# Kernel optimization log

Measured on AMD Instinct MI355X. Metric: run time of the kernel, lower is better.

## Reference

```python
import jax, jax.numpy as jnp
import numpy as np

D = 128
H = 8
HEAD_DIM = D // H
N_NODES = 50000
N_EDGES = 200000
ARGS_PER_EDGE = 3
N_ARGS = N_EDGES * ARGS_PER_EDGE  # 600000
B = N_EDGES // 2                  # 2 edges packed per sequence
S = 2 * (ARGS_PER_EDGE + 1)       # 8
N_TYPES = 512
N_ARGNAMES = 1024


def setup_inputs() -> dict:
    key = jax.random.key(0)
    ks = jax.random.split(key, 10)
    nodes_representations = jax.random.normal(ks[0], (N_NODES, D), jnp.float32)
    hyperedge_arg_node_idxs = jax.random.randint(ks[1], (N_ARGS,), 0, N_NODES)
    unq_hyperedge_type_reprs = jax.random.normal(ks[2], (N_TYPES, D), jnp.float32)
    hyperedge_type_name_unq_idxs = jax.random.randint(ks[3], (N_EDGES,), 0, N_TYPES)
    unq_hyperedge_arg_name_reprs = jax.random.normal(ks[4], (N_ARGNAMES, D), jnp.float32)
    hyperedge_arg_name_unq_idxs = jax.random.randint(ks[5], (N_ARGS,), 0, N_ARGNAMES)

    # Bucket layout: sequence i packs edges e0=2i, e1=2i+1; each edge contributes
    # its 3 arg positions then its state-token position (N_ARGS + edge_id).
    e = np.arange(N_EDGES, dtype=np.int64).reshape(B, 2)          # [B,2]
    arg_base = e * ARGS_PER_EDGE                                   # [B,2]
    per_edge = np.concatenate(
        [arg_base[..., None] + np.arange(ARGS_PER_EDGE), (N_ARGS + e)[..., None]],
        axis=-1)                                                   # [B,2,4]
    flattened_arg_idxs = jnp.asarray(per_edge.reshape(B, S))       # [B,8]
    arg_to_edge_id = jnp.asarray(np.repeat(e, ARGS_PER_EDGE + 1, axis=1))  # [B,8]

    s = 0.05
    W_arg = jax.random.normal(ks[6], (D, D), jnp.float32) * s
    b_arg = jnp.zeros((D,), jnp.float32)
    W_qkv = jax.random.normal(ks[7], (3 * D, D), jnp.float32) * s
    b_qkv = jnp.zeros((3 * D,), jnp.float32)
    W_out = jax.random.normal(ks[8], (D, D), jnp.float32) * s
    b_out = jnp.zeros((D,), jnp.float32)

    return dict(
        nodes_representations=nodes_representations,
        hyperedge_arg_node_idxs=hyperedge_arg_node_idxs,
        unq_hyperedge_type_reprs=unq_hyperedge_type_reprs,
        hyperedge_type_name_unq_idxs=hyperedge_type_name_unq_idxs,
        unq_hyperedge_arg_name_reprs=unq_hyperedge_arg_name_reprs,
        hyperedge_arg_name_unq_idxs=hyperedge_arg_name_unq_idxs,
        flattened_arg_idxs=flattened_arg_idxs,
        arg_to_edge_id=arg_to_edge_id,
        W_arg=W_arg, b_arg=b_arg, W_qkv=W_qkv, b_qkv=b_qkv,
        W_out=W_out, b_out=b_out,
    )


def reference(nodes_representations, hyperedge_arg_node_idxs, unq_hyperedge_type_reprs,
              hyperedge_type_name_unq_idxs, unq_hyperedge_arg_name_reprs,
              hyperedge_arg_name_unq_idxs, flattened_arg_idxs, arg_to_edge_id,
              W_arg, b_arg, W_qkv, b_qkv, W_out, b_out):
    # per-arg representation = gathered node repr + encoded arg-name repr
    arg_name_reprs = (unq_hyperedge_arg_name_reprs @ W_arg.T + b_arg)[hyperedge_arg_name_unq_idxs]
    arg_node_reprs = nodes_representations[hyperedge_arg_node_idxs]
    arg_reprs = arg_node_reprs + arg_name_reprs                       # [N_ARGS, D]
    edge_state_reprs = unq_hyperedge_type_reprs[hyperedge_type_name_unq_idxs]  # [N_EDGES, D]

    # concat args, states, and a trailing ones row (padding target)
    all_reprs = jnp.concatenate(
        [arg_reprs, edge_state_reprs, jnp.ones((1, D), arg_reprs.dtype)], axis=0)  # [L, D]

    x = all_reprs[flattened_arg_idxs]                                 # [B, S, D]

    # torch MultiheadAttention (batch_first, self-attention)
    qkv = x @ W_qkv.T + b_qkv                                         # [B, S, 3D]
    q, k, v = jnp.split(qkv, 3, axis=-1)
    to_heads = lambda t: t.reshape(B, S, H, HEAD_DIM).transpose(0, 2, 1, 3)
    q, k, v = to_heads(q), to_heads(k), to_heads(v)                   # [B, H, S, dh]

    scores = jnp.einsum('bhqd,bhkd->bhqk', q, k) / np.float32(np.sqrt(HEAD_DIM))
    # block-diagonal mask: disallow attention across different edge ids
    mask = arg_to_edge_id[:, :, None] != arg_to_edge_id[:, None, :]   # [B, S, S]
    scores = jnp.where(mask[:, None, :, :], -jnp.inf, scores)
    attn = jax.nn.softmax(scores, axis=-1)
    out = jnp.einsum('bhqk,bhkd->bhqd', attn, v)                      # [B, H, S, dh]
    out = out.transpose(0, 2, 1, 3).reshape(B, S, D)
    messages = out @ W_out.T + b_out                                  # [B, S, D]

    # scatter back into the flat buffer (indices are unique by construction)
    L = N_ARGS + N_EDGES + 1
    buf = jnp.zeros((L, D), messages.dtype)
    buf = buf.at[flattened_arg_idxs.reshape(-1)].set(messages.reshape(-1, D))

    messages_to_nodes = buf[:N_ARGS]
    edge_states = buf[N_ARGS:N_ARGS + N_EDGES]
    return messages_to_nodes, edge_states
```

## Files before the change

### kernel.cpp

```cpp
#include <hip/hip_runtime.h>

#define D        128
#define N_NODES  50000
#define N_EDGES  200000
#define N_ARGS   600000
#define EDGES_PER_TILE 16
#define TOK      64
#define LDX      136

typedef unsigned short u16;
typedef __bf16 bf16x8 __attribute__((ext_vector_type(8)));
typedef float  f32x4  __attribute__((ext_vector_type(4)));

#define MFMA(A,B,C) __builtin_amdgcn_mfma_f32_16x16x32_bf16((A),(B),(C),0,0,0)

#define WS_ARG   0
#define WS_TYPE  262144
#define WS_WQKV  393216
#define WS_WOUT  491520
#define WS_BQKV  524288
#define WS_BOUT  525056
#define WS_FLAG  525312

__device__ __forceinline__ float b2f(u16 h) {
    return __uint_as_float(((unsigned)h) << 16);
}
__device__ __forceinline__ u16 f2b(float f) {
    unsigned u = __float_as_uint(f);
    u += 0x7FFFu + ((u >> 16) & 1u);
    return (u16)(u >> 16);
}
__device__ __forceinline__ unsigned pack2(float lo, float hi) {
    return (unsigned)f2b(lo) | ((unsigned)f2b(hi) << 16);
}
__device__ __forceinline__ unsigned addbf2(unsigned a, unsigned b) {
    float lo = __uint_as_float(a << 16)         + __uint_as_float(b << 16);
    float hi = __uint_as_float(a & 0xFFFF0000u) + __uint_as_float(b & 0xFFFF0000u);
    return pack2(lo, hi);
}

__global__ void sniff_kernel(const u16* __restrict__ probe, int* __restrict__ flag) {
    __shared__ int cnt;
    if (threadIdx.x == 0) cnt = 0;
    __syncthreads();
    float v = b2f(probe[threadIdx.x]);
    float a = fabsf(v);
    int insane = (v != v) || (v != 0.0f && (a < 1e-5f || a > 1e5f));
    atomicAdd(&cnt, insane);
    __syncthreads();
    if (threadIdx.x == 0) *flag = (cnt > 16) ? 1 : 0;
}

__global__ void conv_kernel(const void* __restrict__ t,  const void* __restrict__ wq,
                            const void* __restrict__ wo, const void* __restrict__ bq,
                            const void* __restrict__ bo, char* __restrict__ wsc,
                            const int* __restrict__ flagp) {
    const bool f32 = (*flagp) != 0;
    int i = blockIdx.x * 256 + threadIdx.x;
    const void* src; u16* dst; int j;
    if      (i <  65536) { src = t;  dst = (u16*)(wsc + WS_TYPE); j = i; }
    else if (i < 114688) { src = wq; dst = (u16*)(wsc + WS_WQKV); j = i - 65536; }
    else if (i < 131072) { src = wo; dst = (u16*)(wsc + WS_WOUT); j = i - 114688; }
    else if (i < 131456) { src = bq; dst = (u16*)(wsc + WS_BQKV); j = i - 131072; }
    else if (i < 131584) { src = bo; dst = (u16*)(wsc + WS_BOUT); j = i - 131456; }
    else return;
    dst[j] = f32 ? f2b(((const float*)src)[j]) : ((const u16*)src)[j];
}

__global__ void argname_kernel(const void* __restrict__ unq, const void* __restrict__ W,
                               const void* __restrict__ b, u16* __restrict__ tab,
                               const int* __restrict__ flagp) {
    const bool f32 = (*flagp) != 0;
    int n = blockIdx.x;
    int d = threadIdx.x;
    __shared__ float xs[D];
    xs[d] = f32 ? ((const float*)unq)[n * D + d] : b2f(((const u16*)unq)[n * D + d]);
    __syncthreads();
    float acc = f32 ? ((const float*)b)[d] : b2f(((const u16*)b)[d]);
    if (f32) {
        const float4* wr = (const float4*)((const float*)W + d * D);
        #pragma unroll
        for (int t = 0; t < 32; ++t) {
            float4 wv = wr[t];
            const float* x = &xs[t * 4];
            acc += x[0] * wv.x + x[1] * wv.y + x[2] * wv.z + x[3] * wv.w;
        }
    } else {
        const uint4* wr = (const uint4*)((const u16*)W + d * D);
        #pragma unroll
        for (int t = 0; t < 16; ++t) {
            uint4 wv = wr[t];
            const float* x = &xs[t * 8];
            acc += x[0] * b2f((u16)(wv.x)) + x[1] * b2f((u16)(wv.x >> 16));
            acc += x[2] * b2f((u16)(wv.y)) + x[3] * b2f((u16)(wv.y >> 16));
            acc += x[4] * b2f((u16)(wv.z)) + x[5] * b2f((u16)(wv.z >> 16));
            acc += x[6] * b2f((u16)(wv.w)) + x[7] * b2f((u16)(wv.w >> 16));
        }
    }
    tab[n * D + d] = f2b(acc);
}

__global__ __launch_bounds__(256, 2)
void fused_kernel(const void* __restrict__ nodes,
                  const int*  __restrict__ nidx,
                  const int*  __restrict__ tidx,
                  const int*  __restrict__ anidx,
                  const char* __restrict__ wsc,
                  void*       __restrict__ outv,
                  const int*  __restrict__ flagp) {
    __shared__ __align__(16) u16 Xs[TOK * LDX];
    __shared__ __align__(16) u16 Os[TOK * LDX];

    const bool f32  = (*flagp) != 0;
    const u16* argtab = (const u16*)(wsc + WS_ARG);
    const u16* typetab= (const u16*)(wsc + WS_TYPE);
    const u16* Wqkv   = (const u16*)(wsc + WS_WQKV);
    const u16* Wout   = (const u16*)(wsc + WS_WOUT);
    const u16* bqkv   = (const u16*)(wsc + WS_BQKV);
    const u16* bout   = (const u16*)(wsc + WS_BOUT);

    const int tid  = threadIdx.x;
    const int tile = blockIdx.x;

    {
        int row  = tid >> 2;
        int part = tid & 3;
        int e    = tile * EDGES_PER_TILE + (row >> 2);
        int i    = row & 3;
        uint4* dst = (uint4*)&Xs[row * LDX + part * 32];
        if (i < 3) {
            int a = 3 * e + i;
            const uint4* pa = (const uint4*)(argtab + (long)anidx[a] * D + part * 32);
            if (f32) {
                const float4* pn = (const float4*)((const float*)nodes + (long)nidx[a] * D + part * 32);
                #pragma unroll
                for (int t = 0; t < 4; ++t) {
                    float4 f0 = pn[2 * t], f1 = pn[2 * t + 1];
                    uint4 ua = pa[t], r;
                    r.x = pack2(f0.x + b2f((u16)ua.x), f0.y + b2f((u16)(ua.x >> 16)));
                    r.y = pack2(f0.z + b2f((u16)ua.y), f0.w + b2f((u16)(ua.y >> 16)));
                    r.z = pack2(f1.x + b2f((u16)ua.z), f1.y + b2f((u16)(ua.z >> 16)));
                    r.w = pack2(f1.z + b2f((u16)ua.w), f1.w + b2f((u16)(ua.w >> 16)));
                    dst[t] = r;
                }
            } else {
                const uint4* pn = (const uint4*)((const u16*)nodes + (long)nidx[a] * D + part * 32);
                #pragma unroll
                for (int t = 0; t < 4; ++t) {
                    uint4 un = pn[t], ua = pa[t], r;
                    r.x = addbf2(un.x, ua.x); r.y = addbf2(un.y, ua.y);
                    r.z = addbf2(un.z, ua.z); r.w = addbf2(un.w, ua.w);
                    dst[t] = r;
                }
            }
        } else {
            const uint4* pt = (const uint4*)(typetab + (long)tidx[e] * D + part * 32);
            #pragma unroll
            for (int t = 0; t < 4; ++t) dst[t] = pt[t];
        }
    }
    __syncthreads();

    const int w    = tid >> 6;
    const int lane = tid & 63;
    const int q    = lane >> 4;
    const int c    = lane & 15;

    bf16x8 a[4][4];
    #pragma unroll
    for (int mt = 0; mt < 4; ++mt)
        #pragma unroll
        for (int kk = 0; kk < 4; ++kk)
            a[mt][kk] = *(const bf16x8*)&Xs[(mt * 16 + c) * LDX + kk * 32 + q * 8];

    const f32x4 zero = {0.f, 0.f, 0.f, 0.f};
    const bool valid = (q == (c >> 2));

    #pragma unroll
    for (int hi = 0; hi < 2; ++hi) {
        int h = 2 * w + hi;

        f32x4 QT[4], KT[4], Vv[4];
        {
            f32x4 q0, k0, v0;
            const u16* p0 = bqkv +       h * 16 + q * 4;
            const u16* p1 = bqkv + 128 + h * 16 + q * 4;
            float bv = b2f(bqkv[256 + h * 16 + c]);
            #pragma unroll
            for (int j = 0; j < 4; ++j) {
                q0[j] = b2f(p0[j]); k0[j] = b2f(p1[j]); v0[j] = bv;
            }
            #pragma unroll
            for (int mt = 0; mt < 4; ++mt) { QT[mt] = q0; KT[mt] = k0; Vv[mt] = v0; }
        }

        #pragma unroll
        for (int kk = 0; kk < 4; ++kk) {
            int ko = kk * 32 + q * 8;
            bf16x8 bq = *(const bf16x8*)(Wqkv + (long)(      h * 16 + c) * D + ko);
            bf16x8 bk = *(const bf16x8*)(Wqkv + (long)(128 + h * 16 + c) * D + ko);
            bf16x8 bv = *(const bf16x8*)(Wqkv + (long)(256 + h * 16 + c) * D + ko);
            #pragma unroll
            for (int mt = 0; mt < 4; ++mt) {
                QT[mt] = MFMA(bq, a[mt][kk], QT[mt]);
                KT[mt] = MFMA(bk, a[mt][kk], KT[mt]);
                Vv[mt] = MFMA(a[mt][kk], bv, Vv[mt]);
            }
        }

        #pragma unroll
        for (int mt = 0; mt < 4; ++mt) {
            bf16x8 qf = {}, kf = {}, vf = {};
            #pragma unroll
            for (int j = 0; j < 4; ++j) {
                qf[j] = (__bf16)QT[mt][j];
                kf[j] = (__bf16)KT[mt][j];
                vf[j] = (__bf16)Vv[mt][j];
            }
            f32x4 ST = MFMA(kf, qf, zero);
            float m0 = fmaxf(fmaxf(ST[0], ST[1]), fmaxf(ST[2], ST[3]));
            float e0 = __expf((ST[0] - m0) * 0.25f);
            float e1 = __expf((ST[1] - m0) * 0.25f);
            float e2 = __expf((ST[2] - m0) * 0.25f);
            float e3 = __expf((ST[3] - m0) * 0.25f);
            float inv = 1.0f / (e0 + e1 + e2 + e3);
            bf16x8 pf = {};
            pf[0] = (__bf16)(valid ? e0 * inv : 0.0f);
            pf[1] = (__bf16)(valid ? e1 * inv : 0.0f);
            pf[2] = (__bf16)(valid ? e2 * inv : 0.0f);
            pf[3] = (__bf16)(valid ? e3 * inv : 0.0f);
            f32x4 O = MFMA(pf, vf, zero);
            #pragma unroll
            for (int r = 0; r < 4; ++r)
                Os[(mt * 16 + q * 4 + r) * LDX + h * 16 + c] = f2b(O[r]);
        }
    }
    __syncthreads();

    bf16x8 ao[4][4];
    #pragma unroll
    for (int mt = 0; mt < 4; ++mt)
        #pragma unroll
        for (int kk = 0; kk < 4; ++kk)
            ao[mt][kk] = *(const bf16x8*)&Os[(mt * 16 + c) * LDX + kk * 32 + q * 8];

    #pragma unroll
    for (int hi = 0; hi < 2; ++hi) {
        int nt = 2 * w + hi;
        float bo = b2f(bout[nt * 16 + c]);
        f32x4 acc[4];
        #pragma unroll
        for (int mt = 0; mt < 4; ++mt) {
            #pragma unroll
            for (int r = 0; r < 4; ++r) acc[mt][r] = bo;
        }
        #pragma unroll
        for (int kk = 0; kk < 4; ++kk) {
            bf16x8 bw = *(const bf16x8*)(Wout + (long)(nt * 16 + c) * D + kk * 32 + q * 8);
            #pragma unroll
            for (int mt = 0; mt < 4; ++mt) acc[mt] = MFMA(ao[mt][kk], bw, acc[mt]);
        }
        #pragma unroll
        for (int mt = 0; mt < 4; ++mt)
            #pragma unroll
            for (int r = 0; r < 4; ++r)
                Xs[(mt * 16 + q * 4 + r) * LDX + nt * 16 + c] = f2b(acc[mt][r]);
    }
    __syncthreads();

    {
        int row  = tid >> 2;
        int part = tid & 3;
        int e    = tile * EDGES_PER_TILE + (row >> 2);
        int i    = row & 3;
        long drow = (i < 3) ? (long)(3 * e + i) : (long)(N_ARGS + e);
        const uint4* sp = (const uint4*)&Xs[row * LDX + part * 32];
        if (f32) {
            float4* dp = (float4*)((float*)outv + drow * D + part * 32);
            #pragma unroll
            for (int t = 0; t < 4; ++t) {
                uint4 u = sp[t];
                float4 g0, g1;
                g0.x = b2f((u16)u.x); g0.y = b2f((u16)(u.x >> 16));
                g0.z = b2f((u16)u.y); g0.w = b2f((u16)(u.y >> 16));
                g1.x = b2f((u16)u.z); g1.y = b2f((u16)(u.z >> 16));
                g1.z = b2f((u16)u.w); g1.w = b2f((u16)(u.w >> 16));
                dp[2 * t]     = g0;
                dp[2 * t + 1] = g1;
            }
        } else {
            uint4* dp = (uint4*)((u16*)outv + drow * D + part * 32);
            #pragma unroll
            for (int t = 0; t < 4; ++t) dp[t] = sp[t];
        }
    }
}

extern "C" void kernel_launch(void* const* d_in, const int* in_sizes, int n_in,
                              void* d_out, int out_size, void* d_ws, size_t ws_size,
                              hipStream_t stream) {
    const void* nodes   = d_in[0];
    const int*  nidx    = (const int*)d_in[1];
    const void* typetab = d_in[2];
    const int*  tidx    = (const int*)d_in[3];
    const void* unq_arg = d_in[4];
    const int*  anidx   = (const int*)d_in[5];
    const void* W_arg   = d_in[8];
    const void* b_arg   = d_in[9];
    const void* W_qkv   = d_in[10];
    const void* b_qkv   = d_in[11];
    const void* W_out   = d_in[12];
    const void* b_out   = d_in[13];

    char* wsc   = (char*)d_ws;
    int*  flagp = (int*)(wsc + WS_FLAG);

    sniff_kernel<<<dim3(1), dim3(128), 0, stream>>>((const u16*)nodes, flagp);
    conv_kernel<<<dim3(514), dim3(256), 0, stream>>>(typetab, W_qkv, W_out, b_qkv, b_out,
                                                     wsc, flagp);
    argname_kernel<<<dim3(1024), dim3(128), 0, stream>>>(unq_arg, W_arg, b_arg,
                                                         (u16*)(wsc + WS_ARG), flagp);
    fused_kernel<<<dim3(N_EDGES / EDGES_PER_TILE), dim3(256), 0, stream>>>(
        nodes, nidx, tidx, anidx, wsc, d_out, flagp);
}
```

Measured before the change: 714.4 us.

## Merge prep kernels, write output projection directly from MFMA registers

The sniff, weight-conversion and arg-name projection kernels are combined into one prep kernel, and every block recomputes the dtype flag locally, which removes two launches. In the fused kernel the output projection swaps its MFMA operands so each lane holds four contiguous output columns. Those results are stored straight to global memory, skipping the LDS staging buffer and a barrier. The change also raises the occupancy hint to 4 blocks per SM and uses the hardware bf16 conversion instead of manual rounding. The direct stores are narrower and more scattered than the previous 16-byte row writes, and the higher occupancy hint may force register spills.

```diff
diff --git a/kernel.cpp b/kernel.cpp
--- a/kernel.cpp
+++ b/kernel.cpp
@@ -26,9 +26,8 @@
     return __uint_as_float(((unsigned)h) << 16);
 }
 __device__ __forceinline__ u16 f2b(float f) {
-    unsigned u = __float_as_uint(f);
-    u += 0x7FFFu + ((u >> 16) & 1u);
-    return (u16)(u >> 16);
+    __bf16 h = (__bf16)f;
+    return __builtin_bit_cast(u16, h);
 }
 __device__ __forceinline__ unsigned pack2(float lo, float hi) {
     return (unsigned)f2b(lo) | ((unsigned)f2b(hi) << 16);
@@ -39,68 +38,71 @@
     return pack2(lo, hi);
 }
 
-__global__ void sniff_kernel(const u16* __restrict__ probe, int* __restrict__ flag) {
+__global__ void prep_kernel(const u16*  __restrict__ probe,
+                            const void* __restrict__ t,  const void* __restrict__ wq,
+                            const void* __restrict__ wo, const void* __restrict__ bq,
+                            const void* __restrict__ bo,
+                            const void* __restrict__ unq, const void* __restrict__ Wa,
+                            const void* __restrict__ ba,
+                            char* __restrict__ wsc) {
     __shared__ int cnt;
-    if (threadIdx.x == 0) cnt = 0;
+    __shared__ float xs[2][D];
+    const int tid = threadIdx.x;
+    if (tid == 0) cnt = 0;
     __syncthreads();
-    float v = b2f(probe[threadIdx.x]);
-    float a = fabsf(v);
-    int insane = (v != v) || (v != 0.0f && (a < 1e-5f || a > 1e5f));
-    atomicAdd(&cnt, insane);
+    if (tid < 128) {
+        float v = b2f(probe[tid]);
+        float a = fabsf(v);
+        if ((v != v) || (v != 0.0f && (a < 1e-5f || a > 1e5f))) atomicAdd(&cnt, 1);
+    }
     __syncthreads();
-    if (threadIdx.x == 0) *flag = (cnt > 16) ? 1 : 0;
-}
-
-__global__ void conv_kernel(const void* __restrict__ t,  const void* __restrict__ wq,
-                            const void* __restrict__ wo, const void* __restrict__ bq,
-                            const void* __restrict__ bo, char* __restrict__ wsc,
-                            const int* __restrict__ flagp) {
-    const bool f32 = (*flagp) != 0;
-    int i = blockIdx.x * 256 + threadIdx.x;
-    const void* src; u16* dst; int j;
-    if      (i <  65536) { src = t;  dst = (u16*)(wsc + WS_TYPE); j = i; }
-    else if (i < 114688) { src = wq; dst = (u16*)(wsc + WS_WQKV); j = i - 65536; }
-    else if (i < 131072) { src = wo; dst = (u16*)(wsc + WS_WOUT); j = i - 114688; }
-    else if (i < 131456) { src = bq; dst = (u16*)(wsc + WS_BQKV); j = i - 131072; }
-    else if (i < 131584) { src = bo; dst = (u16*)(wsc + WS_BOUT); j = i - 131456; }
-    else return;
-    dst[j] = f32 ? f2b(((const float*)src)[j]) : ((const u16*)src)[j];
-}
-
-__global__ void argname_kernel(const void* __restrict__ unq, const void* __restrict__ W,
-                               const void* __restrict__ b, u16* __restrict__ tab,
-                               const int* __restrict__ flagp) {
-    const bool f32 = (*flagp) != 0;
-    int n = blockIdx.x;
-    int d = threadIdx.x;
-    __shared__ float xs[D];
-    xs[d] = f32 ? ((const float*)unq)[n * D + d] : b2f(((const u16*)unq)[n * D + d]);
-    __syncthreads();
-    float acc = f32 ? ((const float*)b)[d] : b2f(((const u16*)b)[d]);
-    if (f32) {
-        const float4* wr = (const float4*)((const float*)W + d * D);
-        #pragma unroll
-        for (int t = 0; t < 32; ++t) {
-            float4 wv = wr[t];
-            const float* x = &xs[t * 4];
-            acc += x[0] * wv.x + x[1] * wv.y + x[2] * wv.z + x[3] * wv.w;
-        }
+    const bool f32 = (cnt > 16);
+    if (blockIdx.x == 0 && tid == 0) *(int*)(wsc + WS_FLAG) = f32 ? 1 : 0;
+
+    if (blockIdx.x < 514) {
+        int i = blockIdx.x * 256 + tid;
+        const void* src; u16* dst; int j;
+        if      (i <  65536) { src = t;  dst = (u16*)(wsc + WS_TYPE); j = i; }
+        else if (i < 114688) { src = wq; dst = (u16*)(wsc + WS_WQKV); j = i - 65536; }
+        else if (i < 131072) { src = wo; dst = (u16*)(wsc + WS_WOUT); j = i - 114688; }
+        else if (i < 131456) { src = bq; dst = (u16*)(wsc + WS_BQKV); j = i - 131072; }
+        else if (i < 131584) { src = bo; dst = (u16*)(wsc + WS_BOUT); j = i - 131456; }
+        else return;
+        dst[j] = f32 ? f2b(((const float*)src)[j]) : ((const u16*)src)[j];
     } else {
-        const uint4* wr = (const uint4*)((const u16*)W + d * D);
-        #pragma unroll
-        for (int t = 0; t < 16; ++t) {
-            uint4 wv = wr[t];
-            const float* x = &xs[t * 8];
-            acc += x[0] * b2f((u16)(wv.x)) + x[1] * b2f((u16)(wv.x >> 16));
-            acc += x[2] * b2f((u16)(wv.y)) + x[3] * b2f((u16)(wv.y >> 16));
-            acc += x[4] * b2f((u16)(wv.z)) + x[5] * b2f((u16)(wv.z >> 16));
-            acc += x[6] * b2f((u16)(wv.w)) + x[7] * b2f((u16)(wv.w >> 16));
-        }
-    }
-    tab[n * D + d] = f2b(acc);
-}
-
-__global__ __launch_bounds__(256, 2)
+        int half = tid >> 7;
+        int n    = (blockIdx.x - 514) * 2 + half;
+        int d    = tid & 127;
+        xs[half][d] = f32 ? ((const float*)unq)[n * D + d]
+                          : b2f(((const u16*)unq)[n * D + d]);
+        __syncthreads();
+        float acc = f32 ? ((const float*)ba)[d] : b2f(((const u16*)ba)[d]);
+        const float* x = xs[half];
+        if (f32) {
+            const float4* wr = (const float4*)((const float*)Wa + d * D);
+            #pragma unroll
+            for (int tt = 0; tt < 32; ++tt) {
+                float4 wv = wr[tt];
+                const float* xp = &x[tt * 4];
+                acc += xp[0] * wv.x + xp[1] * wv.y + xp[2] * wv.z + xp[3] * wv.w;
+            }
+        } else {
+            const uint4* wr = (const uint4*)((const u16*)Wa + d * D);
+            #pragma unroll
+            for (int tt = 0; tt < 16; ++tt) {
+                uint4 wv = wr[tt];
+                const float* xp = &x[tt * 8];
+                acc += xp[0] * b2f((u16)(wv.x)) + xp[1] * b2f((u16)(wv.x >> 16));
+                acc += xp[2] * b2f((u16)(wv.y)) + xp[3] * b2f((u16)(wv.y >> 16));
+                acc += xp[4] * b2f((u16)(wv.z)) + xp[5] * b2f((u16)(wv.z >> 16));
+                acc += xp[6] * b2f((u16)(wv.w)) + xp[7] * b2f((u16)(wv.w >> 16));
+            }
+        }
+        ((u16*)(wsc + WS_ARG))[n * D + d] = f2b(acc);
+    }
+}
+
+__global__ __launch_bounds__(256, 4)
 void fused_kernel(const void* __restrict__ nodes,
                   const int*  __restrict__ nidx,
                   const int*  __restrict__ tidx,
@@ -244,54 +246,38 @@
         for (int kk = 0; kk < 4; ++kk)
             ao[mt][kk] = *(const bf16x8*)&Os[(mt * 16 + c) * LDX + kk * 32 + q * 8];
 
+    long drow[4];
+    #pragma unroll
+    for (int mt = 0; mt < 4; ++mt) {
+        int e = tile * EDGES_PER_TILE + mt * 4 + (c >> 2);
+        int i = c & 3;
+        drow[mt] = (i < 3) ? (long)(3 * e + i) : (long)(N_ARGS + e);
+    }
+
     #pragma unroll
     for (int hi = 0; hi < 2; ++hi) {
         int nt = 2 * w + hi;
-        float bo = b2f(bout[nt * 16 + c]);
-        f32x4 acc[4];
+        f32x4 binit;
+        #pragma unroll
+        for (int r = 0; r < 4; ++r) binit[r] = b2f(bout[nt * 16 + q * 4 + r]);
+        bf16x8 bw[4];
+        #pragma unroll
+        for (int kk = 0; kk < 4; ++kk)
+            bw[kk] = *(const bf16x8*)(Wout + (long)(nt * 16 + c) * D + kk * 32 + q * 8);
         #pragma unroll
         for (int mt = 0; mt < 4; ++mt) {
-            #pragma unroll
-            for (int r = 0; r < 4; ++r) acc[mt][r] = bo;
-        }
-        #pragma unroll
-        for (int kk = 0; kk < 4; ++kk) {
-            bf16x8 bw = *(const bf16x8*)(Wout + (long)(nt * 16 + c) * D + kk * 32 + q * 8);
-            #pragma unroll
-            for (int mt = 0; mt < 4; ++mt) acc[mt] = MFMA(ao[mt][kk], bw, acc[mt]);
-        }
-        #pragma unroll
-        for (int mt = 0; mt < 4; ++mt)
-            #pragma unroll
-            for (int r = 0; r < 4; ++r)
-                Xs[(mt * 16 + q * 4 + r) * LDX + nt * 16 + c] = f2b(acc[mt][r]);
-    }
-    __syncthreads();
-
-    {
-        int row  = tid >> 2;
-        int part = tid & 3;
-        int e    = tile * EDGES_PER_TILE + (row >> 2);
-        int i    = row & 3;
-        long drow = (i < 3) ? (long)(3 * e + i) : (long)(N_ARGS + e);
-        const uint4* sp = (const uint4*)&Xs[row * LDX + part * 32];
-        if (f32) {
-            float4* dp = (float4*)((float*)outv + drow * D + part * 32);
-            #pragma unroll
-            for (int t = 0; t < 4; ++t) {
-                uint4 u = sp[t];
-                float4 g0, g1;
-                g0.x = b2f((u16)u.x); g0.y = b2f((u16)(u.x >> 16));
-                g0.z = b2f((u16)u.y); g0.w = b2f((u16)(u.y >> 16));
-                g1.x = b2f((u16)u.z); g1.y = b2f((u16)(u.z >> 16));
-                g1.z = b2f((u16)u.w); g1.w = b2f((u16)(u.w >> 16));
-                dp[2 * t]     = g0;
-                dp[2 * t + 1] = g1;
-            }
-        } else {
-            uint4* dp = (uint4*)((u16*)outv + drow * D + part * 32);
-            #pragma unroll
-            for (int t = 0; t < 4; ++t) dp[t] = sp[t];
+            f32x4 acc = binit;
+            #pragma unroll
+            for (int kk = 0; kk < 4; ++kk)
+                acc = MFMA(bw[kk], ao[mt][kk], acc);
+            if (f32) {
+                *(f32x4*)((float*)outv + drow[mt] * D + nt * 16 + q * 4) = acc;
+            } else {
+                unsigned long long pv =
+                    (unsigned long long)pack2(acc[0], acc[1]) |
+                    ((unsigned long long)pack2(acc[2], acc[3]) << 32);
+                *(unsigned long long*)((u16*)outv + drow[mt] * D + nt * 16 + q * 4) = pv;
+            }
         }
     }
 }
@@ -315,11 +301,9 @@
     char* wsc   = (char*)d_ws;
     int*  flagp = (int*)(wsc + WS_FLAG);
 
-    sniff_kernel<<<dim3(1), dim3(128), 0, stream>>>((const u16*)nodes, flagp);
-    conv_kernel<<<dim3(514), dim3(256), 0, stream>>>(typetab, W_qkv, W_out, b_qkv, b_out,
-                                                     wsc, flagp);
-    argname_kernel<<<dim3(1024), dim3(128), 0, stream>>>(unq_arg, W_arg, b_arg,
-                                                         (u16*)(wsc + WS_ARG), flagp);
+    prep_kernel<<<dim3(1026), dim3(256), 0, stream>>>(
+        (const u16*)nodes, typetab, W_qkv, W_out, b_qkv, b_out,
+        unq_arg, W_arg, b_arg, wsc);
     fused_kernel<<<dim3(N_EDGES / EDGES_PER_TILE), dim3(256), 0, stream>>>(
         nodes, nidx, tidx, anidx, wsc, d_out, flagp);
 }
```

Measured after the change: 891.7 us. 1.25x slower.
